# Kernel optimization log

Hardware: AMD Instinct MI355X
Metric: run time of the kernel (lower is better)

## Reference

```python
import jax, jax.numpy as jnp
import numpy as np

NUM_HEADS = 16
HIDDEN = 1024
HEAD_DIM = HIDDEN // NUM_HEADS
LN_EPS = 1e-5


def setup_inputs() -> dict:
    key = jax.random.key(0)
    ks = jax.random.split(key, 10)
    B, S, D = 2, 2048, HIDDEN
    std = 1.0 / np.sqrt(D)
    inp = {
        "hidden_states": jax.random.normal(ks[0], (B, S, D), dtype=jnp.float32),
        "attention_mask": jnp.zeros((B, 1, 1, S), dtype=jnp.float32),
        "Wq": jax.random.normal(ks[1], (D, D), dtype=jnp.float32) * std,
        "bq": jnp.zeros((D,), dtype=jnp.float32),
        "Wk": jax.random.normal(ks[2], (D, D), dtype=jnp.float32) * std,
        "bk": jnp.zeros((D,), dtype=jnp.float32),
        "Wv": jax.random.normal(ks[3], (D, D), dtype=jnp.float32) * std,
        "bv": jnp.zeros((D,), dtype=jnp.float32),
        "Wo": jax.random.normal(ks[4], (D, D), dtype=jnp.float32) * std,
        "bo": jnpp if False else jnp.zeros((D,), dtype=jnp.float32),
        "ln_gamma": jnp.ones((D,), dtype=jnp.float32),
        "ln_beta": jnp.zeros((D,), dtype=jnp.float32),
    }
    return inp


def _mha(x, mask, Wq, bq, Wk, bk, Wv, bv, Wo, bo, ln_gamma, ln_beta):
    B, S, D = x.shape
    H, Hd = NUM_HEADS, HEAD_DIM
    scale = 1.0 / np.sqrt(Hd).astype(np.float32)

    def split_heads(t):  # [B,S,D] -> [B,H,S,Hd]
        return t.reshape(B, S, H, Hd).transpose(0, 2, 1, 3)

    q = split_heads(x @ Wq + bq)
    k = split_heads(x @ Wk + bk)
    v = split_heads(x @ Wv + bv)

    scores = jnp.einsum("bhqd,bhkd->bhqk", q, k) * scale + mask
    probs = jax.nn.softmax(scores, axis=-1)
    ctx = jnp.einsum("bhqk,bhkd->bhqd", probs, v)
    ctx = ctx.transpose(0, 2, 1, 3).reshape(B, S, D)

    out = ctx @ Wo + bo
    resid = out + x
    mu = jnp.mean(resid, axis=-1, keepdims=True)
    var = jnp.var(resid, axis=-1, keepdims=True)
    return (resid - mu) * jax.lax.rsqrt(var + LN_EPS) * ln_gamma + ln_beta


def reference(hidden_states, attention_mask, Wq, bq, Wk, bk, Wv, bv, Wo, bo, ln_gamma, ln_beta):
    return _mha(hidden_states, attention_mask, Wq, bq, Wk, bk, Wv, bv, Wo, bo, ln_gamma, ln_beta)
```

## Files before the change

kernel.cpp:

```cpp
#include <hip/hip_runtime.h>
#include <hip/hip_bf16.h>
#include <stdint.h>

#define NUMH 16
#define HD   64
#define HID  1024
#define SEQ  2048
#define BATCH 2
#define NTOK (BATCH*SEQ)
#define LN_EPS 1e-5f

typedef __attribute__((ext_vector_type(8)))  short  short8;
typedef __attribute__((ext_vector_type(4)))  float  f32x4;
typedef __attribute__((ext_vector_type(16))) float  f32x16;

#define AS1 __attribute__((address_space(1)))
#define AS3 __attribute__((address_space(3)))

__device__ __forceinline__ void gload_lds16(const void* g, void* l) {
  __builtin_amdgcn_global_load_lds((const AS1 void*)g, (AS3 void*)l, 16, 0, 0);
}

__device__ __forceinline__ unsigned short f2bf(float f) {
  union { float f; unsigned u; } v; v.f = f;
  unsigned u = v.u;
  u += 0x7fffu + ((u >> 16) & 1u);
  return (unsigned short)(u >> 16);
}

__device__ __forceinline__ f32x4 mfma16x16x32(short8 a, short8 b, f32x4 c) {
  return __builtin_amdgcn_mfma_f32_16x16x32_bf16(a, b, c, 0, 0, 0);
}
__device__ __forceinline__ f32x16 mfma32x32x16(short8 a, short8 b, f32x16 c) {
  return __builtin_amdgcn_mfma_f32_32x32x16_bf16(a, b, c, 0, 0, 0);
}

__device__ __forceinline__ unsigned cvtpk(float lo, float hi) {
  unsigned r;
  asm("v_cvt_pk_bf16_f32 %0, %1, %2" : "=v"(r) : "v"(lo), "v"(hi));
  return r;
}
__device__ __forceinline__ void perm32swap(unsigned &a, unsigned &b) {
  asm volatile("v_permlane32_swap_b32 %0, %1" : "+v"(a), "+v"(b));
}
__device__ __forceinline__ float xhalf_max(float x) {
  union { float f; unsigned u; } a, b; a.f = x; b.f = x;
  perm32swap(a.u, b.u);
  return fmaxf(a.f, b.f);
}
__device__ __forceinline__ float xhalf_sum(float x) {
  union { float f; unsigned u; } a, b; a.f = x; b.f = x;
  perm32swap(a.u, b.u);
  return a.f + b.f;
}

__global__ void k_conv_x(const float* __restrict__ x, unsigned short* __restrict__ xb) {
  int i = blockIdx.x * blockDim.x + threadIdx.x;
  f32x4 v = ((const f32x4*)x)[i];
  unsigned short* o = xb + i * 4;
  o[0] = f2bf(v[0]); o[1] = f2bf(v[1]); o[2] = f2bf(v[2]); o[3] = f2bf(v[3]);
}

__global__ void k_transw_all(const float* __restrict__ Wq, const float* __restrict__ Wk,
                             const float* __restrict__ Wv, const float* __restrict__ Wo,
                             unsigned short* __restrict__ WqkvT, unsigned short* __restrict__ WoT) {
  __shared__ float t[32][33];
  int z = blockIdx.z;
  const float* in = (z == 0) ? Wq : (z == 1) ? Wk : (z == 2) ? Wv : Wo;
  unsigned short* out = (z < 3) ? WqkvT + (size_t)z * HID * HID : WoT;
  int tx = threadIdx.x, ty = threadIdx.y;
  int x0 = blockIdx.x * 32, y0 = blockIdx.y * 32;
  for (int j = 0; j < 32; j += 8)
    t[ty + j][tx] = in[(y0 + ty + j) * HID + x0 + tx];
  __syncthreads();
  for (int j = 0; j < 32; j += 8)
    out[(x0 + ty + j) * HID + y0 + tx] = f2bf(t[tx][ty + j]);
}

template<int MODE>
__global__ __launch_bounds__(256, 2)
void k_gemm(const unsigned short* __restrict__ A, const unsigned short* __restrict__ BT,
            int M, int N, int K,
            const float* __restrict__ bias0, const float* __restrict__ bias1,
            const float* __restrict__ bias2, const float* __restrict__ resid,
            unsigned short* __restrict__ outQ, unsigned short* __restrict__ outK,
            unsigned short* __restrict__ outV, float* __restrict__ outF) {
  const int tid  = threadIdx.x;
  const int lane = tid & 63, wave = tid >> 6;
  const int l15 = lane & 15, lhi = lane >> 4;
  const int row0 = blockIdx.x * 128, col0 = blockIdx.y * 128;
  const int wrow = (wave >> 1) * 64, wcol = (wave & 1) * 64;

  __shared__ unsigned short As[128 * 32];
  __shared__ unsigned short Bs[128 * 32];

  f32x4 acc[4][4] = {};

  for (int kt = 0; kt < K; kt += 32) {
    #pragma unroll
    for (int c = 0; c < 2; ++c) {
      int base = wave * 1024 + c * 4096;
      int o = base + lane * 16;
      int r = o >> 6, cb = o & 63;
      gload_lds16(A  + (size_t)(row0 + r) * K + kt + (cb >> 1), As + (base >> 1));
      gload_lds16(BT + (size_t)(col0 + r) * K + kt + (cb >> 1), Bs + (base >> 1));
    }
    __syncthreads();

    short8 af[4], bf[4];
    #pragma unroll
    for (int m = 0; m < 4; ++m)
      af[m] = *(const short8*)(As + (wrow + m * 16 + l15) * 32 + lhi * 8);
    #pragma unroll
    for (int n = 0; n < 4; ++n)
      bf[n] = *(const short8*)(Bs + (wcol + n * 16 + l15) * 32 + lhi * 8);
    #pragma unroll
    for (int m = 0; m < 4; ++m)
      #pragma unroll
      for (int n = 0; n < 4; ++n)
        acc[m][n] = mfma16x16x32(af[m], bf[n], acc[m][n]);
    __syncthreads();
  }

  #pragma unroll
  for (int m = 0; m < 4; ++m)
    #pragma unroll
    for (int n = 0; n < 4; ++n) {
      int col = col0 + wcol + n * 16 + l15;
      #pragma unroll
      for (int j = 0; j < 4; ++j) {
        int row = row0 + wrow + m * 16 + lhi * 4 + j;
        float v = acc[m][n][j];
        if (MODE == 0) {
          int proj = col >> 10, d = col & 1023;
          int h = d >> 6, hd = d & 63;
          int b = row >> 11, s = row & 2047;
          const float* bias = (proj == 0) ? bias0 : (proj == 1) ? bias1 : bias2;
          unsigned short* dst = (proj == 0) ? outQ : (proj == 1) ? outK : outV;
          dst[((size_t)((b * NUMH + h) * SEQ + s) << 6) + hd] = f2bf(v + bias[d]);
        } else {
          size_t idx = (size_t)row * N + col;
          outF[idx] = v + bias0[col] + resid[idx];
        }
      }
    }
}

__global__ void k_vtrans(const unsigned short* __restrict__ V, unsigned short* __restrict__ VT) {
  __shared__ unsigned short t[64][65];
  int bh = blockIdx.y, s0 = blockIdx.x * 64;
  int tid = threadIdx.x;
  for (int it = 0; it < 16; ++it) {
    int idx = it * 256 + tid;
    int r = idx >> 6, c = idx & 63;
    t[r][c] = V[(size_t)(bh * SEQ + s0 + r) * 64 + c];
  }
  __syncthreads();
  for (int it = 0; it < 16; ++it) {
    int idx = it * 256 + tid;
    int d = idx >> 6, sl = idx & 63;
    VT[(size_t)(bh * 64 + d) * SEQ + s0 + sl] = t[sl][d];
  }
}

__global__ __launch_bounds__(256, 2)
void k_attn(const unsigned short* __restrict__ Q, const unsigned short* __restrict__ Kk,
            const unsigned short* __restrict__ VT, const float* __restrict__ mask,
            unsigned short* __restrict__ ctx) {
  const int tid = threadIdx.x, lane = tid & 63, wave = tid >> 6;
  const int l31 = lane & 31, hi = lane >> 5;
  const int bh = blockIdx.x, b = bh >> 4, h = bh & 15;
  const int qs = blockIdx.y * 128 + wave * 32;

  __shared__ __align__(16) unsigned short Ks[2][64 * 64];
  __shared__ __align__(16) unsigned short Vs[2][64 * 64];
  __shared__ __align__(16) float sLds[4][32];

  short8 qf[4];
  {
    const unsigned short* qrow = Q + ((size_t)bh * SEQ + qs + l31) * 64 + hi * 8;
    #pragma unroll
    for (int ks = 0; ks < 4; ++ks) qf[ks] = *(const short8*)(qrow + ks * 16);
  }

  f32x16 o0 = {}, o1 = {};
  float mr = -3.0e38f, lr = 0.f;
  const float LOG2E = 1.44269504088896340736f;
  const float scale = 0.125f;
  const int sw = (l31 & 7) << 4;

  auto stage = [&](int bufi, int kt) {
    #pragma unroll
    for (int c = 0; c < 2; ++c) {
      int base = wave * 1024 + c * 4096;
      int off = base + lane * 16;
      int r = off >> 7, cb = off & 127;
      int scb = cb ^ ((r & 7) << 4);
      gload_lds16(Kk + ((size_t)bh * SEQ + kt + r) * 64 + (scb >> 1), &Ks[bufi][base >> 1]);
      gload_lds16(VT + ((size_t)bh * 64 + r) * SEQ + kt + (scb >> 1), &Vs[bufi][base >> 1]);
    }
  };

  stage(0, 0);
  __syncthreads();
  int cur = 0;

  for (int kt = 0; kt < SEQ; kt += 64) {
    if (kt + 64 < SEQ) stage(cur ^ 1, kt + 64);

    const unsigned short* Kc = Ks[cur];
    const unsigned short* Vc = Vs[cur];
    f32x16 s0 = {}, s1 = {};
    #pragma unroll
    for (int ks = 0; ks < 4; ++ks) {
      int cb = ((ks * 16 + hi * 8) * 2) ^ sw;
      short8 k0 = *(const short8*)((const char*)Kc + l31 * 128 + cb);
      short8 k1 = *(const short8*)((const char*)Kc + (32 + l31) * 128 + cb);
      s0 = mfma32x32x16(k0, qf[ks], s0);
      s1 = mfma32x32x16(k1, qf[ks], s1);
    }

    f32x4 mk0[4], mk1[4];
    #pragma unroll
    for (int rq = 0; rq < 4; ++rq) {
      mk0[rq] = *(const f32x4*)(mask + b * SEQ + kt + rq * 8 + hi * 4);
      mk1[rq] = *(const f32x4*)(mask + b * SEQ + kt + 32 + rq * 8 + hi * 4);
    }
    #pragma unroll
    for (int r = 0; r < 16; ++r) {
      s0[r] = fmaf(s0[r], scale, mk0[r >> 2][r & 3]);
      s1[r] = fmaf(s1[r], scale, mk1[r >> 2][r & 3]);
    }

    float tmax = fmaxf(s0[0], s1[0]);
    #pragma unroll
    for (int r = 1; r < 16; ++r) tmax = fmaxf(tmax, fmaxf(s0[r], s1[r]));
    tmax = xhalf_max(tmax);

    if (!__all(tmax <= mr + 8.0f)) {
      float mnew = fmaxf(mr, tmax);
      float alpha = exp2f((mr - mnew) * LOG2E);
      mr = mnew; lr *= alpha;
      if (hi == 0) sLds[wave][l31] = alpha;
      f32x4 av[4];
      #pragma unroll
      for (int rq = 0; rq < 4; ++rq) av[rq] = *(const f32x4*)&sLds[wave][rq * 8 + hi * 4];
      #pragma unroll
      for (int r = 0; r < 16; ++r) {
        o0[r] *= av[r >> 2][r & 3];
        o1[r] *= av[r >> 2][r & 3];
      }
    }

    float mL = mr * LOG2E;
    float rs = 0.f;
    #pragma unroll
    for (int r = 0; r < 16; ++r) {
      float p0 = exp2f(fmaf(s0[r], LOG2E, -mL));
      float p1 = exp2f(fmaf(s1[r], LOG2E, -mL));
      s0[r] = p0; s1[r] = p1; rs += p0 + p1;
    }
    lr += xhalf_sum(rs);

    unsigned pw[4][4];
    #pragma unroll
    for (int ks = 0; ks < 4; ++ks) {
      int ro = 8 * (ks & 1);
      unsigned a0, a1, b0, b1;
      if (ks < 2) {
        a0 = cvtpk(s0[ro + 0], s0[ro + 1]); a1 = cvtpk(s0[ro + 2], s0[ro + 3]);
        b0 = cvtpk(s0[ro + 4], s0[ro + 5]); b1 = cvtpk(s0[ro + 6], s0[ro + 7]);
      } else {
        a0 = cvtpk(s1[ro + 0], s1[ro + 1]); a1 = cvtpk(s1[ro + 2], s1[ro + 3]);
        b0 = cvtpk(s1[ro + 4], s1[ro + 5]); b1 = cvtpk(s1[ro + 6], s1[ro + 7]);
      }
      perm32swap(a0, b0);
      perm32swap(a1, b1);
      pw[ks][0] = a0; pw[ks][1] = a1; pw[ks][2] = b0; pw[ks][3] = b1;
    }

    #pragma unroll
    for (int ks = 0; ks < 4; ++ks) {
      union { unsigned u[4]; short8 s; } pu;
      pu.u[0] = pw[ks][0]; pu.u[1] = pw[ks][1]; pu.u[2] = pw[ks][2]; pu.u[3] = pw[ks][3];
      int cb = ((ks * 16 + hi * 8) * 2) ^ sw;
      short8 v0 = *(const short8*)((const char*)Vc + l31 * 128 + cb);
      short8 v1 = *(const short8*)((const char*)Vc + (32 + l31) * 128 + cb);
      o0 = mfma32x32x16(pu.s, v0, o0);
      o1 = mfma32x32x16(pu.s, v1, o1);
    }

    __syncthreads();
    cur ^= 1;
  }

  if (hi == 0) sLds[wave][l31] = lr;
  f32x4 lv[4];
  #pragma unroll
  for (int rq = 0; rq < 4; ++rq) {
    f32x4 t = *(const f32x4*)&sLds[wave][rq * 8 + hi * 4];
    lv[rq][0] = 1.f / t[0]; lv[rq][1] = 1.f / t[1];
    lv[rq][2] = 1.f / t[2]; lv[rq][3] = 1.f / t[3];
  }
  #pragma unroll
  for (int r = 0; r < 16; ++r) {
    int q = qs + (r & 3) + 8 * (r >> 2) + 4 * hi;
    float inv = lv[r >> 2][r & 3];
    unsigned short* dst = ctx + (size_t)(b * SEQ + q) * HID + h * 64;
    dst[l31]      = f2bf(o0[r] * inv);
    dst[32 + l31] = f2bf(o1[r] * inv);
  }
}

__global__ __launch_bounds__(256)
void k_ln(const float* __restrict__ resid, const float* __restrict__ gamma,
          const float* __restrict__ beta, float* __restrict__ out) {
  int row = blockIdx.x, tid = threadIdx.x;
  f32x4 v = ((const f32x4*)(resid + (size_t)row * HID))[tid];
  float s = v[0] + v[1] + v[2] + v[3];
  float ss = v[0]*v[0] + v[1]*v[1] + v[2]*v[2] + v[3]*v[3];
  #pragma unroll
  for (int off = 1; off < 64; off <<= 1) { s += __shfl_xor(s, off); ss += __shfl_xor(ss, off); }
  __shared__ float sb[4], ssb[4];
  int wave = tid >> 6, lane = tid & 63;
  if (lane == 0) { sb[wave] = s; ssb[wave] = ss; }
  __syncthreads();
  float ts = sb[0] + sb[1] + sb[2] + sb[3];
  float tss = ssb[0] + ssb[1] + ssb[2] + ssb[3];
  float mu = ts * (1.f / HID);
  float var = tss * (1.f / HID) - mu * mu;
  float rstd = rsqrtf(var + LN_EPS);
  f32x4 g = ((const f32x4*)gamma)[tid];
  f32x4 be = ((const f32x4*)beta)[tid];
  f32x4 o;
  #pragma unroll
  for (int i = 0; i < 4; ++i) o[i] = (v[i] - mu) * rstd * g[i] + be[i];
  ((f32x4*)(out + (size_t)row * HID))[tid] = o;
}

extern "C" void kernel_launch(void* const* d_in, const int* in_sizes, int n_in,
                              void* d_out, int out_size, void* d_ws, size_t ws_size,
                              hipStream_t stream) {
  const float* x     = (const float*)d_in[0];
  const float* mask  = (const float*)d_in[1];
  const float* Wq    = (const float*)d_in[2];
  const float* bq    = (const float*)d_in[3];
  const float* Wk    = (const float*)d_in[4];
  const float* bk    = (const float*)d_in[5];
  const float* Wv    = (const float*)d_in[6];
  const float* bv    = (const float*)d_in[7];
  const float* Wo    = (const float*)d_in[8];
  const float* bo    = (const float*)d_in[9];
  const float* gamma = (const float*)d_in[10];
  const float* beta  = (const float*)d_in[11];
  float* out = (float*)d_out;

  char* w = (char*)d_ws;
  unsigned short* xb    = (unsigned short*)w; w += (size_t)NTOK * HID * 2;
  unsigned short* WqkvT = (unsigned short*)w; w += (size_t)3 * HID * HID * 2;
  unsigned short* WoT   = (unsigned short*)w; w += (size_t)HID * HID * 2;
  unsigned short* Qh    = (unsigned short*)w; w += (size_t)NTOK * HID * 2;
  unsigned short* Kh    = (unsigned short*)w; w += (size_t)NTOK * HID * 2;
  unsigned short* Vh    = (unsigned short*)w; w += (size_t)NTOK * HID * 2;
  unsigned short* VTh   = (unsigned short*)w; w += (size_t)NTOK * HID * 2;
  unsigned short* ctxb  = (unsigned short*)w; w += (size_t)NTOK * HID * 2;
  float*          attn  = (float*)w;          w += (size_t)NTOK * HID * 4;
  (void)ws_size; (void)in_sizes; (void)n_in; (void)out_size;

  k_conv_x<<<NTOK * HID / 4 / 256, 256, 0, stream>>>(x, xb);
  k_transw_all<<<dim3(32, 32, 4), dim3(32, 8), 0, stream>>>(Wq, Wk, Wv, Wo, WqkvT, WoT);

  k_gemm<0><<<dim3(NTOK / 128, 3 * HID / 128), 256, 0, stream>>>(
      xb, WqkvT, NTOK, 3 * HID, HID, bq, bk, bv, nullptr, Qh, Kh, Vh, nullptr);

  k_vtrans<<<dim3(SEQ / 64, BATCH * NUMH), 256, 0, stream>>>(Vh, VTh);

  k_attn<<<dim3(BATCH * NUMH, SEQ / 128), 256, 0, stream>>>(Qh, Kh, VTh, mask, ctxb);

  k_gemm<1><<<dim3(NTOK / 128, HID / 128), 256, 0, stream>>>(
      ctxb, WoT, NTOK, HID, HID, bo, nullptr, nullptr, x, nullptr, nullptr, nullptr, attn);

  k_ln<<<NTOK, 256, 0, stream>>>(attn, gamma, beta, out);
}
```

Before: 233.8 us.

## Merge prep kernels, double GEMM k-tile, remap blocks per XCD, prioritize MFMA

Merges the x conversion and weight transpose into a single prep launch, which saves one kernel launch. The GEMM k-step grows from 32 to 64, halving the number of barriers per output tile at the cost of doubling LDS per block. GEMM blocks are now launched on a 1D grid and remapped so that blocks landing on the same XCD share row and column tiles, which is meant to improve L2 reuse. The attention MFMA sections are wrapped in s_setprio so waves in the matmul phases get issue priority over waves doing softmax.

```diff
diff --git a/kernel.cpp b/kernel.cpp
--- a/kernel.cpp
+++ b/kernel.cpp
@@ -54,21 +54,27 @@
   return a.f + b.f;
 }
 
-__global__ void k_conv_x(const float* __restrict__ x, unsigned short* __restrict__ xb) {
-  int i = blockIdx.x * blockDim.x + threadIdx.x;
-  f32x4 v = ((const f32x4*)x)[i];
-  unsigned short* o = xb + i * 4;
-  o[0] = f2bf(v[0]); o[1] = f2bf(v[1]); o[2] = f2bf(v[2]); o[3] = f2bf(v[3]);
-}
-
-__global__ void k_transw_all(const float* __restrict__ Wq, const float* __restrict__ Wk,
-                             const float* __restrict__ Wv, const float* __restrict__ Wo,
-                             unsigned short* __restrict__ WqkvT, unsigned short* __restrict__ WoT) {
+__global__ void k_prep(const float* __restrict__ Wq, const float* __restrict__ Wk,
+                       const float* __restrict__ Wv, const float* __restrict__ Wo,
+                       const float* __restrict__ x,
+                       unsigned short* __restrict__ WqkvT, unsigned short* __restrict__ WoT,
+                       unsigned short* __restrict__ xb) {
+  int z = blockIdx.z;
+  int tx = threadIdx.x, ty = threadIdx.y;
+  if (z == 4) {
+    int tid = ty * 32 + tx;
+    size_t i0 = ((size_t)(blockIdx.y * 32 + blockIdx.x) * 256 + tid) * 4;
+    #pragma unroll
+    for (int u = 0; u < 4; ++u) {
+      f32x4 v = ((const f32x4*)x)[i0 + u];
+      unsigned short* o = xb + (i0 + u) * 4;
+      o[0] = f2bf(v[0]); o[1] = f2bf(v[1]); o[2] = f2bf(v[2]); o[3] = f2bf(v[3]);
+    }
+    return;
+  }
   __shared__ float t[32][33];
-  int z = blockIdx.z;
   const float* in = (z == 0) ? Wq : (z == 1) ? Wk : (z == 2) ? Wv : Wo;
   unsigned short* out = (z < 3) ? WqkvT + (size_t)z * HID * HID : WoT;
-  int tx = threadIdx.x, ty = threadIdx.y;
   int x0 = blockIdx.x * 32, y0 = blockIdx.y * 32;
   for (int j = 0; j < 32; j += 8)
     t[ty + j][tx] = in[(y0 + ty + j) * HID + x0 + tx];
@@ -88,37 +94,45 @@
   const int tid  = threadIdx.x;
   const int lane = tid & 63, wave = tid >> 6;
   const int l15 = lane & 15, lhi = lane >> 4;
-  const int row0 = blockIdx.x * 128, col0 = blockIdx.y * 128;
+  const int orig = blockIdx.x;
+  const int xcd = orig & 7, i2 = orig >> 3;
+  const int rb  = (xcd & 3) * 8 + (i2 & 7);
+  const int cb2 = (MODE == 0) ? (xcd >> 2) * 12 + (i2 >> 3)
+                              : (xcd >> 2) * 4  + (i2 >> 3);
+  const int row0 = rb * 128, col0 = cb2 * 128;
   const int wrow = (wave >> 1) * 64, wcol = (wave & 1) * 64;
 
-  __shared__ unsigned short As[128 * 32];
-  __shared__ unsigned short Bs[128 * 32];
+  __shared__ unsigned short As[128 * 64];
+  __shared__ unsigned short Bs[128 * 64];
 
   f32x4 acc[4][4] = {};
 
-  for (int kt = 0; kt < K; kt += 32) {
-    #pragma unroll
-    for (int c = 0; c < 2; ++c) {
+  for (int kt = 0; kt < K; kt += 64) {
+    #pragma unroll
+    for (int c = 0; c < 4; ++c) {
       int base = wave * 1024 + c * 4096;
       int o = base + lane * 16;
-      int r = o >> 6, cb = o & 63;
+      int r = o >> 7, cb = o & 127;
       gload_lds16(A  + (size_t)(row0 + r) * K + kt + (cb >> 1), As + (base >> 1));
       gload_lds16(BT + (size_t)(col0 + r) * K + kt + (cb >> 1), Bs + (base >> 1));
     }
     __syncthreads();
 
-    short8 af[4], bf[4];
-    #pragma unroll
-    for (int m = 0; m < 4; ++m)
-      af[m] = *(const short8*)(As + (wrow + m * 16 + l15) * 32 + lhi * 8);
-    #pragma unroll
-    for (int n = 0; n < 4; ++n)
-      bf[n] = *(const short8*)(Bs + (wcol + n * 16 + l15) * 32 + lhi * 8);
-    #pragma unroll
-    for (int m = 0; m < 4; ++m)
+    #pragma unroll
+    for (int kk = 0; kk < 2; ++kk) {
+      short8 af[4], bf[4];
+      #pragma unroll
+      for (int m = 0; m < 4; ++m)
+        af[m] = *(const short8*)(As + (wrow + m * 16 + l15) * 64 + kk * 32 + lhi * 8);
       #pragma unroll
       for (int n = 0; n < 4; ++n)
-        acc[m][n] = mfma16x16x32(af[m], bf[n], acc[m][n]);
+        bf[n] = *(const short8*)(Bs + (wcol + n * 16 + l15) * 64 + kk * 32 + lhi * 8);
+      #pragma unroll
+      for (int m = 0; m < 4; ++m)
+        #pragma unroll
+        for (int n = 0; n < 4; ++n)
+          acc[m][n] = mfma16x16x32(af[m], bf[n], acc[m][n]);
+    }
     __syncthreads();
   }
 
@@ -208,17 +222,20 @@
   for (int kt = 0; kt < SEQ; kt += 64) {
     if (kt + 64 < SEQ) stage(cur ^ 1, kt + 64);
 
-    const unsigned short* Kc = Ks[cur];
-    const unsigned short* Vc = Vs[cur];
+    const char* Kc = (const char*)Ks[cur];
+    const char* Vc = (const char*)Vs[cur];
+
     f32x16 s0 = {}, s1 = {};
+    __builtin_amdgcn_s_setprio(1);
     #pragma unroll
     for (int ks = 0; ks < 4; ++ks) {
       int cb = ((ks * 16 + hi * 8) * 2) ^ sw;
-      short8 k0 = *(const short8*)((const char*)Kc + l31 * 128 + cb);
-      short8 k1 = *(const short8*)((const char*)Kc + (32 + l31) * 128 + cb);
+      short8 k0 = *(const short8*)(Kc + l31 * 128 + cb);
+      short8 k1 = *(const short8*)(Kc + (32 + l31) * 128 + cb);
       s0 = mfma32x32x16(k0, qf[ks], s0);
       s1 = mfma32x32x16(k1, qf[ks], s1);
     }
+    __builtin_amdgcn_s_setprio(0);
 
     f32x4 mk0[4], mk1[4];
     #pragma unroll
@@ -279,16 +296,18 @@
       pw[ks][0] = a0; pw[ks][1] = a1; pw[ks][2] = b0; pw[ks][3] = b1;
     }
 
+    __builtin_amdgcn_s_setprio(1);
     #pragma unroll
     for (int ks = 0; ks < 4; ++ks) {
-      union { unsigned u[4]; short8 s; } pu;
+      union { unsigned u[4]; short8 s8; } pu;
       pu.u[0] = pw[ks][0]; pu.u[1] = pw[ks][1]; pu.u[2] = pw[ks][2]; pu.u[3] = pw[ks][3];
       int cb = ((ks * 16 + hi * 8) * 2) ^ sw;
-      short8 v0 = *(const short8*)((const char*)Vc + l31 * 128 + cb);
-      short8 v1 = *(const short8*)((const char*)Vc + (32 + l31) * 128 + cb);
-      o0 = mfma32x32x16(pu.s, v0, o0);
-      o1 = mfma32x32x16(pu.s, v1, o1);
-    }
+      short8 v0 = *(const short8*)(Vc + l31 * 128 + cb);
+      short8 v1 = *(const short8*)(Vc + (32 + l31) * 128 + cb);
+      o0 = mfma32x32x16(pu.s8, v0, o0);
+      o1 = mfma32x32x16(pu.s8, v1, o1);
+    }
+    __builtin_amdgcn_s_setprio(0);
 
     __syncthreads();
     cur ^= 1;
@@ -367,17 +386,16 @@
   float*          attn  = (float*)w;          w += (size_t)NTOK * HID * 4;
   (void)ws_size; (void)in_sizes; (void)n_in; (void)out_size;
 
-  k_conv_x<<<NTOK * HID / 4 / 256, 256, 0, stream>>>(x, xb);
-  k_transw_all<<<dim3(32, 32, 4), dim3(32, 8), 0, stream>>>(Wq, Wk, Wv, Wo, WqkvT, WoT);
-
-  k_gemm<0><<<dim3(NTOK / 128, 3 * HID / 128), 256, 0, stream>>>(
+  k_prep<<<dim3(32, 32, 5), dim3(32, 8), 0, stream>>>(Wq, Wk, Wv, Wo, x, WqkvT, WoT, xb);
+
+  k_gemm<0><<<768, 256, 0, stream>>>(
       xb, WqkvT, NTOK, 3 * HID, HID, bq, bk, bv, nullptr, Qh, Kh, Vh, nullptr);
 
   k_vtrans<<<dim3(SEQ / 64, BATCH * NUMH), 256, 0, stream>>>(Vh, VTh);
 
   k_attn<<<dim3(BATCH * NUMH, SEQ / 128), 256, 0, stream>>>(Qh, Kh, VTh, mask, ctxb);
 
-  k_gemm<1><<<dim3(NTOK / 128, HID / 128), 256, 0, stream>>>(
+  k_gemm<1><<<256, 256, 0, stream>>>(
       ctxb, WoT, NTOK, HID, HID, bo, nullptr, nullptr, x, nullptr, nullptr, nullptr, attn);
 
   k_ln<<<NTOK, 256, 0, stream>>>(attn, gamma, beta, out);
```

Result: slower. 239.0 us (+2.2%).
